# Kernel tuning notes

Measured on AMD Instinct MI355X. Metric: run time of the kernel, lower is better.

The kernel has to match this reference:

```python
import jax, jax.numpy as jnp
import numpy as np


def setup_inputs() -> dict:
    key = jax.random.key(0)
    k1, k2 = jax.random.split(key)
    bsz, beam_size, step, n = 256, 4, 511, 3
    R = bsz * beam_size          # 1024 hypothesis rows
    L = step + 1                 # 512 tokens generated so far
    V = 50257                    # vocab size
    tokens = jax.random.randint(k1, (R, L), 0, 100, dtype=jnp.int64)
    lprobs = jax.random.normal(k2, (R, V), dtype=jnp.float32)
    return {
        "tokens": tokens,
        "lprobs": lprobs,
        "bsz": bsz,
        "step": step,
        "beam_size": beam_size,
        "no_repeat_ngram_size": n,
    }


def reference(tokens, lprobs, bsz, step, beam_size, no_repeat_ngram_size):
    """Block repeated n-grams: for every row (hypothesis), find all earlier
    (n-1)-grams equal to the trailing (n-1) tokens and set lprobs of the
    token that followed each match to -inf (same math as the CUDA kernel)."""
    n = no_repeat_ngram_size  # static Python int
    R, V = lprobs.shape
    if step + 2 - n <= 0:
        return lprobs  # not enough history yet; kernel is a no-op
    K = step - n + 2                      # number of candidate n-gram starts
    last = tokens[:, step - n + 2:step + 1]           # [R, n-1] trailing context
    starts = jnp.arange(K)
    win_idx = starts[:, None] + jnp.arange(n - 1)[None, :]  # [K, n-1]
    windows = tokens[:, win_idx]                      # [R, K, n-1]
    banned = tokens[:, starts + n - 1]                # [R, K] token after each n-gram
    match = jnp.all(windows == last[:, None, :], axis=-1)   # [R, K]
    rows = jnp.arange(R)[:, None]
    mask = jnp.zeros((R, V), dtype=bool).at[rows, banned].max(match)  # scatter-or
    return jnp.where(mask, -jnp.inf, lprobs)
```

## Files before the change

kernel.cpp:

```cpp
#include <hip/hip_runtime.h>
#include <math.h>

#define NEG_BIG (-3.0e38f)

#define SEGS 4

typedef float v4f __attribute__((ext_vector_type(4)));

__global__ __launch_bounds__(256) void ngram_fused_kernel(
    const void* __restrict__ tokens_raw,
    const float* __restrict__ in,
    float*       __restrict__ out,
    const int*   __restrict__ p_bsz,
    const int*   __restrict__ p_step,
    const int*   __restrict__ p_beam,
    const int*   __restrict__ p_n,
    long long out_elems)
{
    const int bsz  = *p_bsz;
    const int step = *p_step;
    const int beam = *p_beam;
    const int n    = *p_n;

    const int R = bsz * beam;
    const int L = step + 1;
    const long long V = out_elems / R;
    const int K = step - n + 2;
    const int last_base = step - n + 2;

    const int*       t32 = (const int*)tokens_raw;
    const long long* t64 = (const long long*)tokens_raw;
    const int lane = threadIdx.x & 63;
    const int probe_i = (lane < L) ? (2 * lane + 1) : 1;
    const bool odd_nonzero = (t32[probe_i] != 0);
    const bool is64 = (__ballot(odd_nonzero) == 0ULL);

    const int tid = threadIdx.x;
    const int nthreads = blockDim.x;

    const long long seg_len = (V + SEGS - 1) / SEGS;
    const long long total_work = (long long)R * SEGS;

    for (long long work = blockIdx.x; work < total_work; work += gridDim.x) {
        const int row = (int)(work / SEGS);
        const int seg = (int)(work % SEGS);
        const long long s0 = (long long)seg * seg_len;
        long long s1 = s0 + seg_len; if (s1 > V) s1 = V;
        if (s0 >= s1) continue;
        const long long rowbase = (long long)row * V;

        const long long g0 = rowbase + s0;
        const long long g1 = rowbase + s1;
        long long ga = (g0 + 3) & ~3LL; if (ga > g1) ga = g1;
        long long gv = g1 & ~3LL;       if (gv < ga) gv = ga;

        if (tid < (int)(ga - g0)) out[g0 + tid] = in[g0 + tid];
        {
            const v4f* iv = (const v4f*)(in + ga);
            v4f*       ov = (v4f*)(out + ga);
            const long long nv = (gv - ga) >> 2;
            for (long long i = tid; i < nv; i += nthreads) {
                v4f v = __builtin_nontemporal_load(&iv[i]);
                __builtin_nontemporal_store(v, &ov[i]);
            }
        }
        if (tid < (int)(g1 - gv)) out[gv + tid] = in[gv + tid];

        if (K > 0) {
            __syncthreads();
            const long long rb = (long long)row * L;
            for (int k = tid; k < K; k += nthreads) {
                bool match = true;
                for (int j = 0; j < n - 1; ++j) {
                    const int a = is64 ? (int)t64[rb + k + j]         : t32[rb + k + j];
                    const int b = is64 ? (int)t64[rb + last_base + j] : t32[rb + last_base + j];
                    match = match && (a == b);
                }
                if (match) {
                    const long long banned =
                        is64 ? (long long)t64[rb + k + n - 1] : (long long)t32[rb + k + n - 1];
                    if (banned >= s0 && banned < s1) {
                        out[rowbase + banned] = NEG_BIG;
                    }
                }
            }
            __syncthreads();
        }
    }
}

extern "C" void kernel_launch(void* const* d_in, const int* in_sizes, int n_in,
                              void* d_out, int out_size, void* d_ws, size_t ws_size,
                              hipStream_t stream) {
    const void*  tokens = d_in[0];
    const float* lprobs = (const float*)d_in[1];
    const int*   p_bsz  = (const int*)d_in[2];
    const int*   p_step = (const int*)d_in[3];
    const int*   p_beam = (const int*)d_in[4];
    const int*   p_n    = (const int*)d_in[5];
    float* out = (float*)d_out;

    ngram_fused_kernel<<<4096, 256, 0, stream>>>(tokens, lprobs, out,
                                                 p_bsz, p_step, p_beam, p_n,
                                                 (long long)out_size);
}
```

Measured before the change: 359.5 us.

## Build shared-memory ban bitmap before copy and apply mask during streaming

```diff
diff --git a/kernel.cpp b/kernel.cpp
--- a/kernel.cpp
+++ b/kernel.cpp
@@ -3,7 +3,8 @@
 
 #define NEG_BIG (-3.0e38f)
 
-#define SEGS 4
+#define MAX_SEG_COLS 16384
+#define MAX_BM_WORDS (MAX_SEG_COLS / 32)
 
 typedef float v4f __attribute__((ext_vector_type(4)));
 
@@ -17,6 +18,9 @@
     const int*   __restrict__ p_n,
     long long out_elems)
 {
+    __shared__ unsigned int bm[MAX_BM_WORDS + 2];
+    __shared__ int s_any;
+
     const int bsz  = *p_bsz;
     const int step = *p_step;
     const int beam = *p_beam;
@@ -32,42 +36,29 @@
     const long long* t64 = (const long long*)tokens_raw;
     const int lane = threadIdx.x & 63;
     const int probe_i = (lane < L) ? (2 * lane + 1) : 1;
-    const bool odd_nonzero = (t32[probe_i] != 0);
-    const bool is64 = (__ballot(odd_nonzero) == 0ULL);
+    const bool is64 = (__ballot(t32[probe_i] != 0) == 0ULL);
 
     const int tid = threadIdx.x;
     const int nthreads = blockDim.x;
 
-    const long long seg_len = (V + SEGS - 1) / SEGS;
-    const long long total_work = (long long)R * SEGS;
+    const int nseg = (int)((V + MAX_SEG_COLS - 1) / MAX_SEG_COLS);
+    const long long seg_len = (V + nseg - 1) / nseg;
+    const int nwords = (int)((seg_len + 31) >> 5);
+    const long long total_work = (long long)R * nseg;
 
     for (long long work = blockIdx.x; work < total_work; work += gridDim.x) {
-        const int row = (int)(work / SEGS);
-        const int seg = (int)(work % SEGS);
+        const int row = (int)(work / nseg);
+        const int seg = (int)(work % nseg);
         const long long s0 = (long long)seg * seg_len;
         long long s1 = s0 + seg_len; if (s1 > V) s1 = V;
         if (s0 >= s1) continue;
         const long long rowbase = (long long)row * V;
 
-        const long long g0 = rowbase + s0;
-        const long long g1 = rowbase + s1;
-        long long ga = (g0 + 3) & ~3LL; if (ga > g1) ga = g1;
-        long long gv = g1 & ~3LL;       if (gv < ga) gv = ga;
-
-        if (tid < (int)(ga - g0)) out[g0 + tid] = in[g0 + tid];
-        {
-            const v4f* iv = (const v4f*)(in + ga);
-            v4f*       ov = (v4f*)(out + ga);
-            const long long nv = (gv - ga) >> 2;
-            for (long long i = tid; i < nv; i += nthreads) {
-                v4f v = __builtin_nontemporal_load(&iv[i]);
-                __builtin_nontemporal_store(v, &ov[i]);
-            }
-        }
-        if (tid < (int)(g1 - gv)) out[gv + tid] = in[gv + tid];
+        for (int w = tid; w < nwords + 2; w += nthreads) bm[w] = 0u;
+        if (tid == 0) s_any = 0;
+        __syncthreads();
 
         if (K > 0) {
-            __syncthreads();
             const long long rb = (long long)row * L;
             for (int k = tid; k < K; k += nthreads) {
                 bool match = true;
@@ -78,14 +69,59 @@
                 }
                 if (match) {
                     const long long banned =
-                        is64 ? (long long)t64[rb + k + n - 1] : (long long)t32[rb + k + n - 1];
+                        is64 ? t64[rb + k + n - 1] : (long long)t32[rb + k + n - 1];
                     if (banned >= s0 && banned < s1) {
-                        out[rowbase + banned] = NEG_BIG;
+                        const int lc = (int)(banned - s0);
+                        atomicOr(&bm[lc >> 5], 1u << (lc & 31));
+                        s_any = 1;
                     }
                 }
             }
-            __syncthreads();
         }
+        __syncthreads();
+
+        const long long g0 = rowbase + s0;
+        const long long g1 = rowbase + s1;
+        long long ga = (g0 + 3) & ~3LL; if (ga > g1) ga = g1;
+        long long gv = g1 & ~3LL;       if (gv < ga) gv = ga;
+        const v4f* iv = (const v4f*)(in + ga);
+        v4f*       ov = (v4f*)(out + ga);
+        const long long nv = (gv - ga) >> 2;
+
+        if (!s_any) {
+            if (tid < (int)(ga - g0)) out[g0 + tid] = in[g0 + tid];
+            for (long long i = tid; i < nv; i += nthreads) {
+                ov[i] = iv[i];
+            }
+            if (tid < (int)(g1 - gv)) out[gv + tid] = in[gv + tid];
+        } else {
+            if (tid < (int)(ga - g0)) {
+                const long long g = g0 + tid;
+                const int lc = (int)(g - g0) + (int)(s0 - s0);
+                const unsigned bit = (bm[lc >> 5] >> (lc & 31)) & 1u;
+                out[g] = bit ? NEG_BIG : in[g];
+            }
+            const int lbase = (int)(ga - g0);
+            for (long long i = tid; i < nv; i += nthreads) {
+                const int lb = lbase + (int)(i << 2);
+                const unsigned long long pair =
+                    ((unsigned long long)bm[(lb >> 5) + 1] << 32) | bm[lb >> 5];
+                const unsigned bits = (unsigned)((pair >> (lb & 31)) & 0xFULL);
+                v4f v = iv[i];
+                if (bits & 1u) v.x = NEG_BIG;
+                if (bits & 2u) v.y = NEG_BIG;
+                if (bits & 4u) v.z = NEG_BIG;
+                if (bits & 8u) v.w = NEG_BIG;
+                ov[i] = v;
+            }
+            if (tid < (int)(g1 - gv)) {
+                const long long g = gv + tid;
+                const int lc = (int)(g - g0);
+                const unsigned bit = (bm[lc >> 5] >> (lc & 31)) & 1u;
+                out[g] = bit ? NEG_BIG : in[g];
+            }
+        }
+        __syncthreads();
     }
 }
 
```

After: 361.4 us. No clear change (+0.5%).
